# Kernel tuning notes

Measured on AMD Instinct MI355X. Metric: run time of the kernel, lower is better.

Reference implementation:

```python
import jax, jax.numpy as jnp
import numpy as np

WINDOW = 11
SIGMA = 1.5
CHANNELS = 3
C1 = 0.01 ** 2
C2 = 0.03 ** 2


def _gaussian_kernel(size=WINDOW, sigma=SIGMA, channels=CHANNELS):
    coords = jnp.arange(size, dtype=jnp.float32) - size // 2
    g = jnp.exp(-coords ** 2 / (2.0 * sigma ** 2))
    g = jnp.outer(g, g)
    g = g / g.sum()
    # depthwise kernel: [C, 1, K, K] (OIHW with feature_group_count=C)
    return jnp.broadcast_to(g[None, None], (channels, 1, size, size))


def _dwconv(x, kernel):
    # x: [N, C, H, W]; SAME padding, depthwise (groups = C)
    pad = WINDOW // 2
    return jax.lax.conv_general_dilated(
        x, kernel,
        window_strides=(1, 1),
        padding=[(pad, pad), (pad, pad)],
        dimension_numbers=('NCHW', 'OIHW', 'NCHW'),
        feature_group_count=CHANNELS,
    )


def setup_inputs() -> dict:
    key = jax.random.key(0)
    k1, k2 = jax.random.split(key)
    shape = (16, 3, 512, 512)
    pred = jax.random.uniform(k1, shape, dtype=jnp.float32)
    target = jax.random.uniform(k2, shape, dtype=jnp.float32)
    return {"pred": pred, "target": target}


def reference(pred, target):
    kernel = _gaussian_kernel().astype(pred.dtype)
    mu_p = _dwconv(pred, kernel)
    mu_t = _dwconv(target, kernel)
    mu_p2 = mu_p * mu_p
    mu_t2 = mu_t * mu_t
    mu_pt = mu_p * mu_t
    sigma_p2 = _dwconv(pred * pred, kernel) - mu_p2
    sigma_t2 = _dwconv(target * target, kernel) - mu_t2
    sigma_pt = _dwconv(pred * target, kernel) - mu_pt
    ssim_map = ((2.0 * mu_pt + C1) * (2.0 * sigma_pt + C2)) / (
        (mu_p2 + mu_t2 + C1) * (sigma_p2 + sigma_t2 + C2)
    )
    return 1.0 - ssim_map.mean()
```

## Files before the change

### kernel.cpp

```cpp
#include <hip/hip_runtime.h>
#include <math.h>

#define IMG_H 512
#define IMG_W 512
#define TILE  32
#define NSLOT 64

#define HALO_R 42
#define HALO_S 52
#define HT_S   52

typedef _Float16 f16x4 __attribute__((ext_vector_type(4)));
typedef _Float16 f16x8 __attribute__((ext_vector_type(8)));
typedef _Float16 h2    __attribute__((ext_vector_type(2)));
typedef float    f32x4 __attribute__((ext_vector_type(4)));

union F16Frag { f16x8 v8; f16x4 v4[2]; };

__global__ __launch_bounds__(256, 6)
void ssim_main(const float* __restrict__ pred, const float* __restrict__ targ,
               double* __restrict__ acc)
{
    __shared__ _Float16 sAB[2][HALO_R][HALO_S];
    __shared__ _Float16 hT[5][TILE][HT_S];
    __shared__ float wtab[16];
    __shared__ float red[4];

    const int tid  = threadIdx.x;
    const int lane = tid & 63;
    const int wave = tid >> 6;
    const int ln   = lane & 15;
    const int lg   = lane >> 4;

    const int tx = blockIdx.x, ty = blockIdx.y, img = blockIdx.z;
    const float* __restrict__ p = pred + (size_t)img * (IMG_H * IMG_W);
    const float* __restrict__ t = targ + (size_t)img * (IMG_H * IMG_W);
    const int gr0 = ty * TILE - 5;
    const int wo  = tx * TILE - 8;

    if (tid < 16) {
        float d = (float)tid - 5.0f;
        wtab[tid] = (tid <= 10) ? 0.26601173f * expf(-d * d * 0.22222222f) : 0.0f;
    }
    for (int i = tid; i < 480; i += 256) {
        int q = i / 96, rem = i % 96;
        int col = rem / 3, pr = rem % 3;
        *(h2*)&hT[q][col][42 + 2 * pr] = h2{(_Float16)0.f, (_Float16)0.f};
    }

    const int gLo = (tx == 0)  ? 2 : 0;
    const int gHi = (tx == 15) ? 9 : 11;
    #pragma unroll
    for (int it = 0; it < 2; ++it) {
        const int i = tid + it * 256;
        if (i < HALO_R * 12) {
            const int r = i / 12, g = i % 12;
            const int gr = gr0 + r;
            float4 pv = {0.f, 0.f, 0.f, 0.f}, tv = {0.f, 0.f, 0.f, 0.f};
            if (gr >= 0 && gr < IMG_H && g >= gLo && g <= gHi) {
                const size_t base = (size_t)gr * IMG_W + (wo + 4 * g);
                pv = *(const float4*)(p + base);
                tv = *(const float4*)(t + base);
            }
            *(f16x4*)&sAB[0][r][4*g] =
                f16x4{(_Float16)pv.x, (_Float16)pv.y, (_Float16)pv.z, (_Float16)pv.w};
            *(f16x4*)&sAB[1][r][4*g] =
                f16x4{(_Float16)tv.x, (_Float16)tv.y, (_Float16)tv.z, (_Float16)tv.w};
        }
    }
    __syncthreads();

    f16x8 Bw, A2w;
    #pragma unroll
    for (int j = 0; j < 8; ++j) {
        int k  = lg * 8 + j;
        int dh = k - ln - 3;
        int dv = k - ln;
        Bw[j]  = (_Float16)(((unsigned)dh <= 10u) ? wtab[dh & 15] : 0.0f);
        A2w[j] = (_Float16)(((unsigned)dv <= 10u) ? wtab[dv & 15] : 0.0f);
    }
    const f32x4 zacc = {0.f, 0.f, 0.f, 0.f};

    for (int tt = wave; tt < 6; tt += 4) {
        const int rt = tt >> 1, ct = tt & 1;
        const int rowbase = (rt == 2) ? 26 : rt * 16;
        const int arow = rowbase + ln;
        const int acol = ct * 16 + lg * 8;
        const int ocol = ct * 16 + ln;
        const int orow = rowbase + lg * 4;
        F16Frag pa, ta;
        pa.v4[0] = *(const f16x4*)&sAB[0][arow][acol];
        pa.v4[1] = *(const f16x4*)&sAB[0][arow][acol + 4];
        ta.v4[0] = *(const f16x4*)&sAB[1][arow][acol];
        ta.v4[1] = *(const f16x4*)&sAB[1][arow][acol + 4];
        f16x8 fq[5];
        fq[0] = pa.v8;
        fq[1] = ta.v8;
        fq[2] = pa.v8 * pa.v8;
        fq[3] = ta.v8 * ta.v8;
        fq[4] = pa.v8 * ta.v8;
        #pragma unroll
        for (int q = 0; q < 5; ++q) {
            f32x4 d = __builtin_amdgcn_mfma_f32_16x16x32_f16(fq[q], Bw, zacc, 0, 0, 0);
            *(h2*)&hT[q][ocol][orow]     = h2{(_Float16)d[0], (_Float16)d[1]};
            *(h2*)&hT[q][ocol][orow + 2] = h2{(_Float16)d[2], (_Float16)d[3]};
        }
    }
    __syncthreads();

    float lsum = 0.f;
    {
        const int ctv = wave & 1, rtv = wave >> 1;
        const int ocol  = ctv * 16 + ln;
        const int rbase = rtv * 16 + lg * 8;
        f32x4 accq[5];
        #pragma unroll
        for (int q = 0; q < 5; ++q) {
            F16Frag b;
            b.v4[0] = *(const f16x4*)&hT[q][ocol][rbase];
            b.v4[1] = *(const f16x4*)&hT[q][ocol][rbase + 4];
            accq[q] = __builtin_amdgcn_mfma_f32_16x16x32_f16(A2w, b.v8, zacc, 0, 0, 0);
        }
        const float C1 = 1e-4f, C2 = 9e-4f;
        #pragma unroll
        for (int rgi = 0; rgi < 4; ++rgi) {
            float mp = accq[0][rgi], mt = accq[1][rgi];
            float vp = accq[2][rgi] - mp * mp;
            float vt = accq[3][rgi] - mt * mt;
            float cv = accq[4][rgi] - mp * mt;
            float num = (2.f * mp * mt + C1) * (2.f * cv + C2);
            float den = (mp * mp + mt * mt + C1) * (vp + vt + C2);
            lsum = fmaf(num, __builtin_amdgcn_rcpf(den), lsum);
        }
    }

    #pragma unroll
    for (int off = 32; off > 0; off >>= 1)
        lsum += __shfl_down(lsum, off, 64);
    if ((tid & 63) == 0) red[wave] = lsum;
    __syncthreads();
    if (tid == 0) {
        float bs = red[0] + red[1] + red[2] + red[3];
        int slot = (blockIdx.z * 256 + blockIdx.y * 16 + blockIdx.x) & (NSLOT - 1);
        atomicAdd(&acc[slot], (double)bs);
    }
}

__global__ void ssim_init(double* acc)
{
    if (threadIdx.x < NSLOT) acc[threadIdx.x] = 0.0;
}

__global__ void ssim_fin(const double* __restrict__ acc, float* __restrict__ out,
                         double inv_n)
{
    if (threadIdx.x == 0) {
        double s = 0.0;
        for (int i = 0; i < NSLOT; ++i) s += acc[i];
        out[0] = (float)(1.0 - s * inv_n);
    }
}

extern "C" void kernel_launch(void* const* d_in, const int* in_sizes, int n_in,
                              void* d_out, int out_size, void* d_ws, size_t ws_size,
                              hipStream_t stream)
{
    const float* pred = (const float*)d_in[0];
    const float* targ = (const float*)d_in[1];
    float* out  = (float*)d_out;
    double* acc = (double*)d_ws;

    const long long total = (long long)in_sizes[0];
    const int n_img = (int)(total / (IMG_H * IMG_W));

    hipLaunchKernelGGL(ssim_init, dim3(1), dim3(64), 0, stream, acc);
    dim3 grid(IMG_W / TILE, IMG_H / TILE, n_img);
    hipLaunchKernelGGL(ssim_main, grid, dim3(256), 0, stream, pred, targ, acc);
    hipLaunchKernelGGL(ssim_fin, dim3(1), dim3(1), 0, stream, acc, out,
                       1.0 / (double)total);
}
```

Baseline: 141.4 us.

## Load inputs directly into MFMA fragments and replace atomics with per-wave partial sums

Removes the shared-memory halo staging buffer. Each wave now loads its fp32 pred/target fragments straight from global memory into registers, which drops one barrier and frees LDS for higher occupancy (launch bound raised to 8). The Gaussian weights are computed in registers with exp2f instead of through a shared table. The block-level reduction and double atomics are replaced by per-wave partial sums written to the workspace and summed by a one-block finalize kernel, so the init kernel is also dropped. In exchange, overlapping halo rows are now fetched redundantly from global memory or cache by different waves, and the loads are less coalesced.

```diff
diff --git a/kernel.cpp b/kernel.cpp
--- a/kernel.cpp
+++ b/kernel.cpp
@@ -5,10 +5,7 @@
 #define IMG_W 512
 #define TILE  32
 #define NSLOT 64
-
-#define HALO_R 42
-#define HALO_S 52
-#define HT_S   52
+#define HT_S  52
 
 typedef _Float16 f16x4 __attribute__((ext_vector_type(4)));
 typedef _Float16 f16x8 __attribute__((ext_vector_type(8)));
@@ -17,14 +14,11 @@
 
 union F16Frag { f16x8 v8; f16x4 v4[2]; };
 
-__global__ __launch_bounds__(256, 6)
+__global__ __launch_bounds__(256, 8)
 void ssim_main(const float* __restrict__ pred, const float* __restrict__ targ,
-               double* __restrict__ acc)
+               float* __restrict__ partial, double* __restrict__ acc, int mode)
 {
-    __shared__ _Float16 sAB[2][HALO_R][HALO_S];
     __shared__ _Float16 hT[5][TILE][HT_S];
-    __shared__ float wtab[16];
-    __shared__ float red[4];
 
     const int tid  = threadIdx.x;
     const int lane = tid & 63;
@@ -38,74 +32,61 @@
     const int gr0 = ty * TILE - 5;
     const int wo  = tx * TILE - 8;
 
-    if (tid < 16) {
-        float d = (float)tid - 5.0f;
-        wtab[tid] = (tid <= 10) ? 0.26601173f * expf(-d * d * 0.22222222f) : 0.0f;
+    if (tid < 160) {
+        int q = tid / 32, col = tid & 31;
+        *(h2*)&hT[q][col][42] = h2{(_Float16)0.f, (_Float16)0.f};
+        *(h2*)&hT[q][col][44] = h2{(_Float16)0.f, (_Float16)0.f};
+        *(h2*)&hT[q][col][46] = h2{(_Float16)0.f, (_Float16)0.f};
     }
-    for (int i = tid; i < 480; i += 256) {
-        int q = i / 96, rem = i % 96;
-        int col = rem / 3, pr = rem % 3;
-        *(h2*)&hT[q][col][42 + 2 * pr] = h2{(_Float16)0.f, (_Float16)0.f};
-    }
-
-    const int gLo = (tx == 0)  ? 2 : 0;
-    const int gHi = (tx == 15) ? 9 : 11;
-    #pragma unroll
-    for (int it = 0; it < 2; ++it) {
-        const int i = tid + it * 256;
-        if (i < HALO_R * 12) {
-            const int r = i / 12, g = i % 12;
-            const int gr = gr0 + r;
-            float4 pv = {0.f, 0.f, 0.f, 0.f}, tv = {0.f, 0.f, 0.f, 0.f};
-            if (gr >= 0 && gr < IMG_H && g >= gLo && g <= gHi) {
-                const size_t base = (size_t)gr * IMG_W + (wo + 4 * g);
-                pv = *(const float4*)(p + base);
-                tv = *(const float4*)(t + base);
-            }
-            *(f16x4*)&sAB[0][r][4*g] =
-                f16x4{(_Float16)pv.x, (_Float16)pv.y, (_Float16)pv.z, (_Float16)pv.w};
-            *(f16x4*)&sAB[1][r][4*g] =
-                f16x4{(_Float16)tv.x, (_Float16)tv.y, (_Float16)tv.z, (_Float16)tv.w};
-        }
-    }
-    __syncthreads();
 
     f16x8 Bw, A2w;
     #pragma unroll
     for (int j = 0; j < 8; ++j) {
         int k  = lg * 8 + j;
-        int dh = k - ln - 3;
-        int dv = k - ln;
-        Bw[j]  = (_Float16)(((unsigned)dh <= 10u) ? wtab[dh & 15] : 0.0f);
-        A2w[j] = (_Float16)(((unsigned)dv <= 10u) ? wtab[dv & 15] : 0.0f);
+        int ih = k - ln - 3;
+        int iv = k - ln;
+        float dh = (float)(ih - 5), dv = (float)(iv - 5);
+        float vh = 0.26601173f * exp2f(-dh * dh * 0.32059889f);
+        float vv = 0.26601173f * exp2f(-dv * dv * 0.32059889f);
+        Bw[j]  = (_Float16)(((unsigned)ih <= 10u) ? vh : 0.0f);
+        A2w[j] = (_Float16)(((unsigned)iv <= 10u) ? vv : 0.0f);
     }
     const f32x4 zacc = {0.f, 0.f, 0.f, 0.f};
 
-    for (int tt = wave; tt < 6; tt += 4) {
+    auto do_tile = [&](int tt) {
         const int rt = tt >> 1, ct = tt & 1;
         const int rowbase = (rt == 2) ? 26 : rt * 16;
-        const int arow = rowbase + ln;
-        const int acol = ct * 16 + lg * 8;
-        const int ocol = ct * 16 + ln;
-        const int orow = rowbase + lg * 4;
+        const int gr = gr0 + rowbase + ln;
+        const int gc = wo + ct * 16 + lg * 8;
+        float4 pv0 = {0,0,0,0}, pv1 = {0,0,0,0}, tv0 = {0,0,0,0}, tv1 = {0,0,0,0};
+        if (gr >= 0 && gr < IMG_H && gc >= 0 && gc <= IMG_W - 8) {
+            const float* bp = p + (size_t)gr * IMG_W + gc;
+            const float* bt = t + (size_t)gr * IMG_W + gc;
+            pv0 = ((const float4*)bp)[0]; pv1 = ((const float4*)bp)[1];
+            tv0 = ((const float4*)bt)[0]; tv1 = ((const float4*)bt)[1];
+        }
         F16Frag pa, ta;
-        pa.v4[0] = *(const f16x4*)&sAB[0][arow][acol];
-        pa.v4[1] = *(const f16x4*)&sAB[0][arow][acol + 4];
-        ta.v4[0] = *(const f16x4*)&sAB[1][arow][acol];
-        ta.v4[1] = *(const f16x4*)&sAB[1][arow][acol + 4];
+        pa.v8 = f16x8{(_Float16)pv0.x, (_Float16)pv0.y, (_Float16)pv0.z, (_Float16)pv0.w,
+                      (_Float16)pv1.x, (_Float16)pv1.y, (_Float16)pv1.z, (_Float16)pv1.w};
+        ta.v8 = f16x8{(_Float16)tv0.x, (_Float16)tv0.y, (_Float16)tv0.z, (_Float16)tv0.w,
+                      (_Float16)tv1.x, (_Float16)tv1.y, (_Float16)tv1.z, (_Float16)tv1.w};
         f16x8 fq[5];
         fq[0] = pa.v8;
         fq[1] = ta.v8;
         fq[2] = pa.v8 * pa.v8;
         fq[3] = ta.v8 * ta.v8;
         fq[4] = pa.v8 * ta.v8;
+        const int ocol = ct * 16 + ln;
+        const int orow = rowbase + lg * 4;
         #pragma unroll
         for (int q = 0; q < 5; ++q) {
             f32x4 d = __builtin_amdgcn_mfma_f32_16x16x32_f16(fq[q], Bw, zacc, 0, 0, 0);
             *(h2*)&hT[q][ocol][orow]     = h2{(_Float16)d[0], (_Float16)d[1]};
             *(h2*)&hT[q][ocol][orow + 2] = h2{(_Float16)d[2], (_Float16)d[3]};
         }
-    }
+    };
+    do_tile(wave);
+    if (wave < 2) do_tile(wave + 4);
     __syncthreads();
 
     float lsum = 0.f;
@@ -137,12 +118,13 @@
     #pragma unroll
     for (int off = 32; off > 0; off >>= 1)
         lsum += __shfl_down(lsum, off, 64);
-    if ((tid & 63) == 0) red[wave] = lsum;
-    __syncthreads();
-    if (tid == 0) {
-        float bs = red[0] + red[1] + red[2] + red[3];
-        int slot = (blockIdx.z * 256 + blockIdx.y * 16 + blockIdx.x) & (NSLOT - 1);
-        atomicAdd(&acc[slot], (double)bs);
+    if ((lane) == 0) {
+        const int bid = (blockIdx.z * gridDim.y + blockIdx.y) * gridDim.x + blockIdx.x;
+        if (mode == 0) {
+            partial[bid * 4 + wave] = lsum;
+        } else {
+            atomicAdd(&acc[(bid * 4 + wave) & (NSLOT - 1)], (double)lsum);
+        }
     }
 }
 
@@ -151,8 +133,28 @@
     if (threadIdx.x < NSLOT) acc[threadIdx.x] = 0.0;
 }
 
-__global__ void ssim_fin(const double* __restrict__ acc, float* __restrict__ out,
-                         double inv_n)
+__global__ __launch_bounds__(256)
+void ssim_fin_slots(const float* __restrict__ partial, float* __restrict__ out,
+                    int n4, double inv_n)
+{
+    __shared__ double red[4];
+    double s = 0.0;
+    const int tid = threadIdx.x;
+    for (int i = tid; i < n4; i += 256) {
+        float4 v = ((const float4*)partial)[i];
+        s += (double)v.x + (double)v.y + (double)v.z + (double)v.w;
+    }
+    #pragma unroll
+    for (int off = 32; off > 0; off >>= 1)
+        s += __shfl_down(s, off, 64);
+    if ((tid & 63) == 0) red[tid >> 6] = s;
+    __syncthreads();
+    if (tid == 0)
+        out[0] = (float)(1.0 - (red[0] + red[1] + red[2] + red[3]) * inv_n);
+}
+
+__global__ void ssim_fin_atomic(const double* __restrict__ acc, float* __restrict__ out,
+                                double inv_n)
 {
     if (threadIdx.x == 0) {
         double s = 0.0;
@@ -167,15 +169,27 @@
 {
     const float* pred = (const float*)d_in[0];
     const float* targ = (const float*)d_in[1];
-    float* out  = (float*)d_out;
-    double* acc = (double*)d_ws;
+    float* out = (float*)d_out;
 
     const long long total = (long long)in_sizes[0];
     const int n_img = (int)(total / (IMG_H * IMG_W));
+    dim3 grid(IMG_W / TILE, IMG_H / TILE, n_img);
+    const int nblk = grid.x * grid.y * grid.z;
+    const int nslots = nblk * 4;
+    const double inv_n = 1.0 / (double)total;
 
-    hipLaunchKernelGGL(ssim_init, dim3(1), dim3(64), 0, stream, acc);
-    dim3 grid(IMG_W / TILE, IMG_H / TILE, n_img);
-    hipLaunchKernelGGL(ssim_main, grid, dim3(256), 0, stream, pred, targ, acc);
-    hipLaunchKernelGGL(ssim_fin, dim3(1), dim3(1), 0, stream, acc, out,
-                       1.0 / (double)total);
+    if (ws_size >= (size_t)nslots * sizeof(float)) {
+        float* partial = (float*)d_ws;
+        hipLaunchKernelGGL(ssim_main, grid, dim3(256), 0, stream,
+                           pred, targ, partial, (double*)nullptr, 0);
+        hipLaunchKernelGGL(ssim_fin_slots, dim3(1), dim3(256), 0, stream,
+                           partial, out, nslots / 4, inv_n);
+    } else {
+        double* acc = (double*)d_ws;
+        hipLaunchKernelGGL(ssim_init, dim3(1), dim3(64), 0, stream, acc);
+        hipLaunchKernelGGL(ssim_main, grid, dim3(256), 0, stream,
+                           pred, targ, (float*)nullptr, acc, 1);
+        hipLaunchKernelGGL(ssim_fin_atomic, dim3(1), dim3(1), 0, stream,
+                           acc, out, inv_n);
+    }
 }
```

Result: slower. 156.4 us (+10.6%).
